# Optimization experiments

Measured on AMD Instinct MI355X. Metric: run time of the kernel, lower is better.

## Reference

```python
import jax, jax.numpy as jnp
import numpy as np

ROTARY_BASE = 10000
INFTY_APPROX = 1e30
B, T, M, H, D = 2, 2048, 2048, 16, 128


def rope(x):
    # x: [B, T, H, D]; half-split rotary encoding
    *_, length, _, width = x.shape
    half = width // 2
    positions = jnp.arange(length, dtype=jnp.float32)[None, :, None, None]      # [1,T,1,1]
    dims = jnp.arange(half, dtype=jnp.float32)
    ang_freqs = jnp.power(float(ROTARY_BASE), -dims / half)[None, None, None, :]  # [1,1,1,D/2]
    radians = positions * ang_freqs
    cos = jnp.cos(radians).astype(x.dtype)
    sin = jnp.sin(radians).astype(x.dtype)
    even, odd = x[..., :half], x[..., half:]
    r_even = even * cos - odd * sin
    r_odd = even * sin + odd * cos
    return jnp.concatenate([r_even, r_odd], axis=-1)


def setup_inputs() -> dict:
    key = jax.random.key(0)
    k0, k1, k2, k3, k4 = jax.random.split(key, 5)
    return {
        "x": jax.random.normal(k0, (B, T, M), dtype=jnp.float32),
        "w_aq": jax.random.normal(k1, (H, M, D), dtype=jnp.float32) * (M ** -0.5),
        "w_ak": jax.random.normal(k2, (H, M, D), dtype=jnp.float32) * (M ** -0.5),
        "w_av": jax.random.normal(k3, (H, M, D), dtype=jnp.float32) * (M ** -0.5),
        "w_ao": jax.random.normal(k4, (H, D, M), dtype=jnp.float32) * ((2 * 24 * M) ** -0.5),
    }


def reference(x, w_aq, w_ak, w_av, w_ao):
    q = jnp.einsum("btm,hmd->bthd", x, w_aq)
    k = jnp.einsum("btm,hmd->bthd", x, w_ak)
    v = jnp.einsum("btm,hmd->bthd", x, w_av)
    q = rope(q)
    k = rope(k)
    # muP attention scaling: 1/d_head (not 1/sqrt(d_head))
    mult = (1.0 / D) ** 0.5
    s = jnp.einsum("bihd,bjhd->bhij", mult * q, mult * k)  # [B,H,T,T]
    i = jnp.arange(T)[:, None]
    j = jnp.arange(T)[None, :]
    mask = (i < j)[None, None, :, :]  # mask future positions
    s = s - jnp.asarray(INFTY_APPROX, dtype=x.dtype) * mask
    p = jax.nn.softmax(s, axis=-1)
    o = jnp.einsum("bhij,bjhd->bihd", p, v)
    r = jnp.einsum("bihd,hdm->bim", o, w_ao)
    return r
```

## Files before the change

### kernel.cpp

```cpp
#include <hip/hip_runtime.h>

#define Bb 2
#define Tt 2048
#define Mm 2048
#define Hh 16
#define Dd 128

typedef __attribute__((ext_vector_type(8))) short bf16x8;
typedef __attribute__((ext_vector_type(4))) float f32x4;
typedef __attribute__((ext_vector_type(16))) float f32x16;

__device__ __forceinline__ unsigned short f2bf(float f) {
    unsigned int u = __builtin_bit_cast(unsigned int, f);
    u += 0x7FFFu + ((u >> 16) & 1u);
    return (unsigned short)(u >> 16);
}

__device__ __forceinline__ unsigned int cvt_pk_bf16(float lo, float hi) {
    unsigned int r;
    asm("v_cvt_pk_bf16_f32 %0, %1, %2" : "=v"(r) : "v"(lo), "v"(hi));
    return r;
}

__device__ __forceinline__ float fexp2(float x) { return __builtin_amdgcn_exp2f(x); }

__device__ __forceinline__ void gld16(const void* g, void* l) {
    __builtin_amdgcn_global_load_lds(
        (const __attribute__((address_space(1))) void*)g,
        (__attribute__((address_space(3))) void*)l, 16, 0, 0);
}


__global__ __launch_bounds__(256) void cvt_x_kernel(const float* __restrict__ x,
                                                    unsigned short* __restrict__ xb) {
    long i = ((long)blockIdx.x * 256 + threadIdx.x) * 4;
    float4 v = *(const float4*)(x + i);
    unsigned short r0 = f2bf(v.x), r1 = f2bf(v.y), r2 = f2bf(v.z), r3 = f2bf(v.w);
    unsigned int lo = (unsigned int)r0 | ((unsigned int)r1 << 16);
    unsigned int hi = (unsigned int)r2 | ((unsigned int)r3 << 16);
    uint2 packed; packed.x = lo; packed.y = hi;
    *(uint2*)(xb + i) = packed;
}

__global__ __launch_bounds__(256) void transpose_cvt(const float* __restrict__ in,
                                                     unsigned short* __restrict__ out,
                                                     int rows, int cols,
                                                     long in_slab, long out_slab) {
    __shared__ float tile[32][33];
    const float* ip = in + (long)blockIdx.z * in_slab;
    unsigned short* op = out + (long)blockIdx.z * out_slab;
    int r0 = blockIdx.x * 32, c0 = blockIdx.y * 32;
    int tx = threadIdx.x & 31, ty = threadIdx.x >> 5;
#pragma unroll
    for (int j = 0; j < 32; j += 8)
        tile[ty + j][tx] = ip[(long)(r0 + ty + j) * cols + c0 + tx];
    __syncthreads();
#pragma unroll
    for (int j = 0; j < 32; j += 8)
        op[(long)(c0 + ty + j) * rows + r0 + tx] = f2bf(tile[tx][ty + j]);
}

__global__ __launch_bounds__(256) void rope_tab(float* __restrict__ cosT,
                                                float* __restrict__ sinT) {
    int idx = blockIdx.x * 256 + threadIdx.x;
    int t = idx >> 6, d = idx & 63;
    float freq = powf(10000.f, -(float)d / 64.f);
    float ang = (float)t * freq;
    sinT[idx] = sinf(ang);
    cosT[idx] = cosf(ang);
}

__global__ __launch_bounds__(256) void proj_gemm(
    const unsigned short* __restrict__ xb,
    const unsigned short* __restrict__ wqT,
    const unsigned short* __restrict__ wkT,
    const unsigned short* __restrict__ wvT,
    unsigned short* __restrict__ qO,
    unsigned short* __restrict__ kO,
    unsigned short* __restrict__ vtO,
    const float* __restrict__ cosT,
    const float* __restrict__ sinT) {
    __shared__ __align__(16) unsigned short smem[32768];

    const int mode = blockIdx.z;
    const unsigned short* wT = (mode == 0) ? wqT : (mode == 1) ? wkT : wvT;
    const int bm = blockIdx.x;
    const int h  = blockIdx.y;
    const int tid = threadIdx.x;
    const int lane = tid & 63;
    const int wave = tid >> 6;
    const int g = lane >> 4;
    const int ln = lane & 15;

    const unsigned short* arow = xb + (long)bm * 128 * Mm;
    const unsigned short* brow = wT + (long)h * 128 * Mm;

    f32x4 acc[2][8];
#pragma unroll
    for (int a = 0; a < 2; ++a)
#pragma unroll
        for (int b2 = 0; b2 < 8; ++b2)
#pragma unroll
            for (int e = 0; e < 4; ++e) acc[a][b2][e] = 0.f;

    auto stage = [&](int buf, int kt) {
        const int k0 = kt * 64;
#pragma unroll
        for (int it = 0; it < 4; ++it) {
            int f = it * 256 + tid;
            int r = f >> 3, c = f & 7;
            long off = (long)r * Mm + k0 + ((c ^ (r & 7)) << 3);
            gld16(arow + off, (char*)smem + buf * 32768 + f * 16);
            gld16(brow + off, (char*)smem + buf * 32768 + 16384 + f * 16);
        }
    };

    stage(0, 0);

    for (int kt = 0; kt < Mm / 64; ++kt) {
        const int cur = kt & 1;
        if (kt + 1 < Mm / 64) {
            stage(cur ^ 1, kt + 1);
            asm volatile("s_waitcnt vmcnt(8)" ::: "memory");
        } else {
            asm volatile("s_waitcnt vmcnt(0)" ::: "memory");
        }
        __builtin_amdgcn_s_barrier();

        const char* Ab = (const char*)smem + cur * 32768;
        const char* Bv = Ab + 16384;
#pragma unroll
        for (int kc = 0; kc < 2; ++kc) {
            bf16x8 af[2];
#pragma unroll
            for (int rf = 0; rf < 2; ++rf) {
                int row = wave * 32 + rf * 16 + ln;
                int byte = (row * 128 + kc * 64 + g * 16) ^ ((row & 7) << 4);
                af[rf] = *(const bf16x8*)(Ab + byte);
            }
#pragma unroll
            for (int ni = 0; ni < 8; ++ni) {
                int row = ni * 16 + ln;
                int byte = (row * 128 + kc * 64 + g * 16) ^ ((row & 7) << 4);
                bf16x8 bfv = *(const bf16x8*)(Bv + byte);
#pragma unroll
                for (int rf = 0; rf < 2; ++rf)
                    acc[rf][ni] = __builtin_amdgcn_mfma_f32_16x16x32_bf16(af[rf], bfv, acc[rf][ni], 0, 0, 0);
            }
        }
        asm volatile("" ::: "memory");
        __builtin_amdgcn_s_barrier();
    }

    const int b  = bm >> 4;
    const int t0 = (bm & 15) * 128;

    if (mode < 2) {
        const float qscale = (mode == 0) ? 0.011271055f : 1.0f;
        unsigned short* out = (mode == 0) ? qO : kO;
        long hb = ((long)(b * Hh + h)) * Tt;
#pragma unroll
        for (int rf = 0; rf < 2; ++rf)
#pragma unroll
            for (int reg = 0; reg < 4; ++reg) {
                int i = wave * 32 + rf * 16 + g * 4 + reg;
                int t = t0 + i;
                long base = (hb + t) * Dd;
#pragma unroll
                for (int ni = 0; ni < 4; ++ni) {
                    int d = ni * 16 + ln;
                    float c = cosT[t * 64 + d];
                    float s = sinT[t * 64 + d];
                    float ev = acc[rf][ni][reg];
                    float od = acc[rf][ni + 4][reg];
                    out[base + d]      = f2bf((ev * c - od * s) * qscale);
                    out[base + d + 64] = f2bf((ev * s + od * c) * qscale);
                }
            }
    } else {
        __syncthreads();
#pragma unroll
        for (int rf = 0; rf < 2; ++rf)
#pragma unroll
            for (int ni = 0; ni < 8; ++ni)
#pragma unroll
                for (int reg = 0; reg < 4; ++reg) {
                    int i = wave * 32 + rf * 16 + g * 4 + reg;
                    int d = ni * 16 + ln;
                    int byte = (d * 256 + i * 2) ^ ((d & 7) << 4);
                    *(unsigned short*)((char*)smem + byte) = f2bf(acc[rf][ni][reg]);
                }
        __syncthreads();
        long hb = ((long)(b * Hh + h)) * Dd;
#pragma unroll
        for (int rep = 0; rep < 8; ++rep) {
            int d = rep * 16 + (tid >> 4);
            int tb = tid & 15;
            int byte = (d * 256 + tb * 16) ^ ((d & 7) << 4);
            uint4 v = *(const uint4*)((char*)smem + byte);
            *(uint4*)(vtO + ((hb + d) * Tt + t0 + tb * 8)) = v;
        }
    }
}

__global__ __launch_bounds__(256) void attn_kernel(
    const unsigned short* __restrict__ q,
    const unsigned short* __restrict__ k,
    const unsigned short* __restrict__ vt,
    unsigned short* __restrict__ o) {
    __shared__ __align__(16) unsigned short lds[32768];

    const int lid = (int)blockIdx.x;
    const int p = lid & 255;
    const int bh = p & 31;
    const int q0 = p >> 5;
    const int qb = (lid >> 8) ? (15 - q0) : q0;

    const int tid = threadIdx.x, lane = tid & 63, wave = tid >> 6;
    const int h = lane >> 5, iln = lane & 31;

    const unsigned short* qp = q + (long)bh * Tt * Dd;
    const unsigned short* kp = k + (long)bh * Tt * Dd;
    const unsigned short* vp = vt + (long)bh * Dd * Tt;

    const int i_g = qb * 128 + wave * 32 + iln;
    bf16x8 qf[8];
#pragma unroll
    for (int kk = 0; kk < 8; ++kk)
        qf[kk] = *(const bf16x8*)(qp + (long)i_g * Dd + kk * 16 + h * 8);

    f32x16 accO[4];
#pragma unroll
    for (int nb = 0; nb < 4; ++nb)
#pragma unroll
        for (int e = 0; e < 16; ++e) accO[nb][e] = 0.f;

    float m_r = -1e30f, l_r = 0.f;

    const int ntiles = 2 * qb + 2;

    auto stage = [&](int buf, int tix) {
        const int j0s = tix * 64;
#pragma unroll
        for (int it = 0; it < 4; ++it) {
            int f = it * 256 + tid;
            int rk = f >> 4, ck = f & 15;
            gld16(kp + ((long)(j0s + rk) * Dd + ((ck ^ (rk & 7)) << 3)),
                  (char*)lds + buf * 16384 + f * 16);
            int rv = f >> 3, cv = f & 7;
            gld16(vp + ((long)rv * Tt + j0s + ((cv ^ (rv & 7)) << 3)),
                  (char*)lds + 32768 + buf * 16384 + f * 16);
        }
    };

    stage(0, 0);

    for (int tix = 0; tix < ntiles; ++tix) {
        const int cur = tix & 1;
        const int j0 = tix * 64;
        if (tix + 1 < ntiles) {
            stage(cur ^ 1, tix + 1);
            asm volatile("s_waitcnt vmcnt(8)" ::: "memory");
        } else {
            asm volatile("s_waitcnt vmcnt(0)" ::: "memory");
        }
        __builtin_amdgcn_s_barrier();

        const char* Kb = (const char*)lds + cur * 16384;
        const char* Vb = (const char*)lds + 32768 + cur * 16384;

        f32x16 sacc[2];
#pragma unroll
        for (int mb = 0; mb < 2; ++mb)
#pragma unroll
            for (int e = 0; e < 16; ++e) sacc[mb][e] = 0.f;

        __builtin_amdgcn_s_setprio(1);
#pragma unroll
        for (int mb = 0; mb < 2; ++mb) {
            int row = mb * 32 + iln;
            const char* Kr = Kb + row * 256;
            int sw = row & 7;
#pragma unroll
            for (int kk = 0; kk < 8; ++kk) {
                bf16x8 kf = *(const bf16x8*)(Kr + 16 * ((kk * 2 + h) ^ sw));
                sacc[mb] = __builtin_amdgcn_mfma_f32_32x32x16_bf16(kf, qf[kk], sacc[mb], 0, 0, 0);
            }
        }
        __builtin_amdgcn_s_setprio(0);

        const bool domask = (j0 + 63 > qb * 128);
        if (domask) {
#pragma unroll
            for (int mb = 0; mb < 2; ++mb)
#pragma unroll
                for (int reg = 0; reg < 16; ++reg) {
                    int j = j0 + mb * 32 + (reg & 3) + 8 * (reg >> 2) + 4 * h;
                    if (j > i_g) sacc[mb][reg] = -1e30f;
                }
        }

        float red[16];
#pragma unroll
        for (int r = 0; r < 16; ++r) red[r] = fmaxf(sacc[0][r], sacc[1][r]);
#pragma unroll
        for (int s = 8; s >= 1; s >>= 1)
#pragma unroll
            for (int r = 0; r < s; ++r) red[r] = fmaxf(red[r], red[r + s]);
        float mx = fmaxf(red[0], __shfl_xor(red[0], 32, 64));

        if (__any(mx > m_r + 8.f)) {
            float mn = fmaxf(m_r, mx);
            float corr = fexp2(m_r - mn);
            m_r = mn;
            l_r *= corr;
#pragma unroll
            for (int reg = 0; reg < 16; ++reg) {
                int rrow = (reg & 3) + 8 * (reg >> 2) + 4 * h;
                float c = __shfl(corr, rrow, 64);
#pragma unroll
                for (int nb = 0; nb < 4; ++nb) accO[nb][reg] *= c;
            }
        }

        float pe[2][16];
#pragma unroll
        for (int mb = 0; mb < 2; ++mb)
#pragma unroll
            for (int r = 0; r < 16; ++r) pe[mb][r] = fexp2(sacc[mb][r] - m_r);
        float sr[16];
#pragma unroll
        for (int r = 0; r < 16; ++r) sr[r] = pe[0][r] + pe[1][r];
#pragma unroll
        for (int s = 8; s >= 1; s >>= 1)
#pragma unroll
            for (int r = 0; r < s; ++r) sr[r] += sr[r + s];
        l_r += sr[0] + __shfl_xor(sr[0], 32, 64);

        unsigned int pu[2][8];
#pragma unroll
        for (int mb = 0; mb < 2; ++mb)
#pragma unroll
            for (int t = 0; t < 8; ++t)
                pu[mb][t] = cvt_pk_bf16(pe[mb][2 * t], pe[mb][2 * t + 1]);

        unsigned int rv[2][4];
#pragma unroll
        for (int mb = 0; mb < 2; ++mb)
#pragma unroll
            for (int u = 0; u < 4; ++u) {
                unsigned int sv = h ? pu[mb][(u & 1) + 4 * (u >> 1)]
                                    : pu[mb][2 + (u & 1) + 4 * (u >> 1)];
                rv[mb][u] = __shfl_xor(sv, 32, 64);
            }

        __builtin_amdgcn_s_setprio(1);
#pragma unroll
        for (int kk2 = 0; kk2 < 4; ++kk2) {
            const int mb = kk2 >> 1, c2 = kk2 & 1;
            unsigned int w0 = h ? rv[mb][2 * c2 + 0] : pu[mb][4 * c2 + 0];
            unsigned int w1 = h ? rv[mb][2 * c2 + 1] : pu[mb][4 * c2 + 1];
            unsigned int w2 = h ? pu[mb][4 * c2 + 2] : rv[mb][2 * c2 + 0];
            unsigned int w3 = h ? pu[mb][4 * c2 + 3] : rv[mb][2 * c2 + 1];
            uint4 aw; aw.x = w0; aw.y = w1; aw.z = w2; aw.w = w3;
            bf16x8 af = __builtin_bit_cast(bf16x8, aw);
#pragma unroll
            for (int nb = 0; nb < 4; ++nb) {
                int d = nb * 32 + iln;
                int byte = d * 128 + 16 * ((kk2 * 2 + h) ^ (d & 7));
                bf16x8 vf = *(const bf16x8*)(Vb + byte);
                accO[nb] = __builtin_amdgcn_mfma_f32_32x32x16_bf16(af, vf, accO[nb], 0, 0, 0);
            }
        }
        __builtin_amdgcn_s_setprio(0);

        asm volatile("" ::: "memory");
        __builtin_amdgcn_s_barrier();
    }

    const int b = bh >> 4, hh = bh & 15;
    float invl = 1.f / l_r;
#pragma unroll
    for (int reg = 0; reg < 16; ++reg) {
        int rrow = (reg & 3) + 8 * (reg >> 2) + 4 * h;
        float iv = __shfl(invl, rrow, 64);
        int t = qb * 128 + wave * 32 + rrow;
        long base = ((long)(b * Tt + t) * Hh + hh) * Dd;
#pragma unroll
        for (int nb = 0; nb < 4; ++nb)
            o[base + nb * 32 + iln] = f2bf(accO[nb][reg] * iv);
    }
}

__global__ __launch_bounds__(256) void out_gemm(
    const unsigned short* __restrict__ oIn,
    const unsigned short* __restrict__ woT,
    float* __restrict__ out) {
    __shared__ __align__(16) unsigned short smem[32768];
    const int bm = blockIdx.x, bn = blockIdx.y;
    const int tid = threadIdx.x;
    const int lane = tid & 63;
    const int wave = tid >> 6;
    const int g = lane >> 4;
    const int ln = lane & 15;

    const unsigned short* arow = oIn + (long)bm * 128 * Mm;
    const unsigned short* brow = woT + (long)bn * 128 * Mm;

    f32x4 acc[2][8];
#pragma unroll
    for (int a = 0; a < 2; ++a)
#pragma unroll
        for (int b2 = 0; b2 < 8; ++b2)
#pragma unroll
            for (int e = 0; e < 4; ++e) acc[a][b2][e] = 0.f;

    auto stage = [&](int buf, int kt) {
        const int k0 = kt * 64;
#pragma unroll
        for (int it = 0; it < 4; ++it) {
            int f = it * 256 + tid;
            int r = f >> 3, c = f & 7;
            long off = (long)r * Mm + k0 + ((c ^ (r & 7)) << 3);
            gld16(arow + off, (char*)smem + buf * 32768 + f * 16);
            gld16(brow + off, (char*)smem + buf * 32768 + 16384 + f * 16);
        }
    };

    stage(0, 0);

    for (int kt = 0; kt < Mm / 64; ++kt) {
        const int cur = kt & 1;
        if (kt + 1 < Mm / 64) {
            stage(cur ^ 1, kt + 1);
            asm volatile("s_waitcnt vmcnt(8)" ::: "memory");
        } else {
            asm volatile("s_waitcnt vmcnt(0)" ::: "memory");
        }
        __builtin_amdgcn_s_barrier();

        const char* Ab = (const char*)smem + cur * 32768;
        const char* Bv = Ab + 16384;
#pragma unroll
        for (int kc = 0; kc < 2; ++kc) {
            bf16x8 af[2];
#pragma unroll
            for (int rf = 0; rf < 2; ++rf) {
                int row = wave * 32 + rf * 16 + ln;
                int byte = (row * 128 + kc * 64 + g * 16) ^ ((row & 7) << 4);
                af[rf] = *(const bf16x8*)(Ab + byte);
            }
#pragma unroll
            for (int ni = 0; ni < 8; ++ni) {
                int row = ni * 16 + ln;
                int byte = (row * 128 + kc * 64 + g * 16) ^ ((row & 7) << 4);
                bf16x8 bfv = *(const bf16x8*)(Bv + byte);
#pragma unroll
                for (int rf = 0; rf < 2; ++rf)
                    acc[rf][ni] = __builtin_amdgcn_mfma_f32_16x16x32_bf16(af[rf], bfv, acc[rf][ni], 0, 0, 0);
            }
        }
        asm volatile("" ::: "memory");
        __builtin_amdgcn_s_barrier();
    }

#pragma unroll
    for (int rf = 0; rf < 2; ++rf)
#pragma unroll
        for (int reg = 0; reg < 4; ++reg) {
            long row = bm * 128 + wave * 32 + rf * 16 + g * 4 + reg;
#pragma unroll
            for (int ni = 0; ni < 8; ++ni)
                out[row * Mm + bn * 128 + ni * 16 + ln] = acc[rf][ni][reg];
        }
}


extern "C" void kernel_launch(void* const* d_in, const int* in_sizes, int n_in,
                              void* d_out, int out_size, void* d_ws, size_t ws_size,
                              hipStream_t stream) {
    const float* x    = (const float*)d_in[0];
    const float* w_aq = (const float*)d_in[1];
    const float* w_ak = (const float*)d_in[2];
    const float* w_av = (const float*)d_in[3];
    const float* w_ao = (const float*)d_in[4];
    float* out = (float*)d_out;

    char* ws = (char*)d_ws;
    const long SZ_BTM = 16777216;
    const long SZ_W   = 8388608;
    unsigned short* xb  = (unsigned short*)(ws);
    unsigned short* qB  = (unsigned short*)(ws + SZ_BTM);
    unsigned short* kB  = (unsigned short*)(ws + 2 * SZ_BTM);
    unsigned short* vtB = (unsigned short*)(ws + 3 * SZ_BTM);
    unsigned short* oB  = (unsigned short*)(ws + 4 * SZ_BTM);
    unsigned short* wqT = (unsigned short*)(ws + 5 * SZ_BTM);
    unsigned short* wkT = (unsigned short*)(ws + 5 * SZ_BTM + SZ_W);
    unsigned short* wvT = (unsigned short*)(ws + 5 * SZ_BTM + 2 * SZ_W);
    unsigned short* woT = (unsigned short*)(ws + 5 * SZ_BTM + 3 * SZ_W);
    float* cosT = (float*)(ws + 5 * SZ_BTM + 4 * SZ_W);
    float* sinT = (float*)(ws + 5 * SZ_BTM + 4 * SZ_W + 524288);

    cvt_x_kernel<<<8192, 256, 0, stream>>>(x, xb);
    transpose_cvt<<<dim3(64, 4, 16), 256, 0, stream>>>(w_aq, wqT, 2048, 128, (long)2048 * 128, (long)128 * 2048);
    transpose_cvt<<<dim3(64, 4, 16), 256, 0, stream>>>(w_ak, wkT, 2048, 128, (long)2048 * 128, (long)128 * 2048);
    transpose_cvt<<<dim3(64, 4, 16), 256, 0, stream>>>(w_av, wvT, 2048, 128, (long)2048 * 128, (long)128 * 2048);
    transpose_cvt<<<dim3(64, 64, 1), 256, 0, stream>>>(w_ao, woT, 2048, 2048, 0, 0);
    rope_tab<<<512, 256, 0, stream>>>(cosT, sinT);

    proj_gemm<<<dim3(32, 16, 3), 256, 0, stream>>>(xb, wqT, wkT, wvT, qB, kB, vtB, cosT, sinT);
    attn_kernel<<<dim3(512), 256, 0, stream>>>(qB, kB, vtB, oB);
    out_gemm<<<dim3(32, 16), 256, 0, stream>>>(oB, woT, out);
}
```

Before: 263.1 us.

## Rewrite QKV projection as 256-row tiles with 512 threads over fused N

Replaces the per-head 128x128 projection GEMM with a 512-thread kernel that computes a 256-row tile against 384 output columns of the concatenated Q/K/V weights, split into 256- and 128-wide subtiles. It uses a two-stage pipeline with 128 KB of LDS and interleaved half-tile loads. The three Q/K/V weight transposes are merged into one launch, and the weight rows are permuted so RoPE even/odd pairs land in matching accumulators. This aims to raise arithmetic intensity and cut A-operand reloads. In exchange it uses far more LDS per block, which limits occupancy, and adds complex indexing and wait-count logic.

Result: faster. 257.7 us (-2.1%).

```diff
diff --git a/kernel.cpp b/kernel.cpp
--- a/kernel.cpp
+++ b/kernel.cpp
@@ -5,6 +5,7 @@
 #define Mm 2048
 #define Hh 16
 #define Dd 128
+#define PROJ_NT 32
 
 typedef __attribute__((ext_vector_type(8))) short bf16x8;
 typedef __attribute__((ext_vector_type(4))) float f32x4;
@@ -60,6 +61,28 @@
         op[(long)(c0 + ty + j) * rows + r0 + tx] = f2bf(tile[tx][ty + j]);
 }
 
+__global__ __launch_bounds__(256) void transpose_cvt_qkv(
+    const float* __restrict__ wq, const float* __restrict__ wk, const float* __restrict__ wv,
+    unsigned short* __restrict__ outBase) {
+    __shared__ float tile[32][33];
+    const int z = blockIdx.z;
+    const int which = z >> 4, slab = z & 15;
+    const float* ip = (which == 0 ? wq : which == 1 ? wk : wv) + (long)slab * 2048 * 128;
+    unsigned short* op = outBase + (long)which * 4194304 + (long)slab * 128 * 2048;
+    int r0 = blockIdx.x * 32, c0 = blockIdx.y * 32;
+    int tx = threadIdx.x & 31, ty = threadIdx.x >> 5;
+#pragma unroll
+    for (int j = 0; j < 32; j += 8)
+        tile[ty + j][tx] = ip[(long)(r0 + ty + j) * 128 + c0 + tx];
+    __syncthreads();
+#pragma unroll
+    for (int j = 0; j < 32; j += 8) {
+        int d = c0 + ty + j;
+        int p = (((d >> 4) & 3) * 2 + (d >> 6)) * 16 + (d & 15);
+        op[(long)p * 2048 + r0 + tx] = f2bf(tile[tx][ty + j]);
+    }
+}
+
 __global__ __launch_bounds__(256) void rope_tab(float* __restrict__ cosT,
                                                 float* __restrict__ sinT) {
     int idx = blockIdx.x * 256 + threadIdx.x;
@@ -70,7 +93,198 @@
     cosT[idx] = cosf(ang);
 }
 
-__global__ __launch_bounds__(256) void proj_gemm(
+template <int BN>
+__device__ __forceinline__ void do_subtile(
+    const unsigned short* __restrict__ Asrc,
+    const unsigned short* __restrict__ Bsrc,
+    char* lds, int mode, int off, int bm,
+    unsigned short* __restrict__ qO, unsigned short* __restrict__ kO,
+    unsigned short* __restrict__ vtO,
+    const float* __restrict__ cosT, const float* __restrict__ sinT,
+    int tid) {
+    const int lane = tid & 63, wave = tid >> 6;
+    const int wm = wave >> 2, wn = wave & 3;
+    const int ln = lane & 15, g4 = lane >> 4;
+    constexpr int NF = BN / 64;
+    constexpr int NQ = (BN == 256) ? 2 : 1;
+
+    f32x4 acc[8][NF];
+#pragma unroll
+    for (int a = 0; a < 8; ++a)
+#pragma unroll
+        for (int b2 = 0; b2 < NF; ++b2)
+#pragma unroll
+            for (int e = 0; e < 4; ++e) acc[a][b2][e] = 0.f;
+
+    auto stA = [&](char* buf, int h, int kt) {
+#pragma unroll
+        for (int l = 0; l < 2; ++l) {
+            int f = l * 512 + tid;
+            int s = ((f >> 9) << 1) + h;
+            int q = f & 511;
+            int r = q >> 3;
+            gld16(Asrc + (long)(s * 64 + r) * Mm + kt * 64 + (((q & 7) ^ (r & 7)) << 3),
+                  buf + s * 8192 + q * 16);
+        }
+    };
+    auto stB = [&](char* buf, int h, int kt) {
+        if constexpr (BN == 256) {
+#pragma unroll
+            for (int l = 0; l < 2; ++l) {
+                int f = l * 512 + tid;
+                int s = ((f >> 8) << 1) + h;
+                int q = f & 255;
+                int r = q >> 3;
+                gld16(Bsrc + (long)(s * 32 + r) * Mm + kt * 64 + (((q & 7) ^ (r & 7)) << 3),
+                      buf + 32768 + s * 4096 + q * 16);
+            }
+        } else {
+            int f = tid;
+            int s = ((f >> 7) << 1) + h;
+            int q = f & 127;
+            int r = q >> 3;
+            gld16(Bsrc + (long)(s * 16 + r) * Mm + kt * 64 + (((q & 7) ^ (r & 7)) << 3),
+                  buf + 32768 + s * 2048 + q * 16);
+        }
+    };
+
+    auto rdA = [&](const char* buf, int MH, int mf, int kk) -> bf16x8 {
+        int row = wm * 128 + MH * 64 + mf * 16 + ln;
+        int byte = (row >> 6) * 8192 + ((((row & 63) * 128) + (kk * 4 + g4) * 16) ^ ((row & 7) << 4));
+        return *(const bf16x8*)(buf + byte);
+    };
+    auto rdB = [&](const char* buf, int NH, int nf, int kk) -> bf16x8 {
+        if constexpr (BN == 256) {
+            int col = wn * 64 + NH * 32 + nf * 16 + ln;
+            int byte = 32768 + (col >> 5) * 4096 +
+                       ((((col & 31) * 128) + (kk * 4 + g4) * 16) ^ ((col & 7) << 4));
+            return *(const bf16x8*)(buf + byte);
+        } else {
+            int col = wn * 32 + NH * 16 + ln;
+            int byte = 32768 + (col >> 4) * 2048 +
+                       ((((col & 15) * 128) + (kk * 4 + g4) * 16) ^ ((col & 7) << 4));
+            return *(const bf16x8*)(buf + byte);
+        }
+    };
+
+    auto phase = [&](const char* bc, int MH, int NH) {
+        bf16x8 af[4][2];
+#pragma unroll
+        for (int mf = 0; mf < 4; ++mf)
+#pragma unroll
+            for (int kk = 0; kk < 2; ++kk) af[mf][kk] = rdA(bc, MH, mf, kk);
+        bf16x8 bfr[NQ][2];
+#pragma unroll
+        for (int nf = 0; nf < NQ; ++nf)
+#pragma unroll
+            for (int kk = 0; kk < 2; ++kk) bfr[nf][kk] = rdB(bc, NH, nf, kk);
+        __builtin_amdgcn_s_setprio(1);
+#pragma unroll
+        for (int mf = 0; mf < 4; ++mf)
+#pragma unroll
+            for (int nf = 0; nf < NQ; ++nf)
+#pragma unroll
+                for (int kk = 0; kk < 2; ++kk)
+                    acc[MH * 4 + mf][NH * NQ + nf] = __builtin_amdgcn_mfma_f32_16x16x32_bf16(
+                        af[mf][kk], bfr[nf][kk], acc[MH * 4 + mf][NH * NQ + nf], 0, 0, 0);
+        __builtin_amdgcn_s_setprio(0);
+    };
+
+    stB(lds, 0, 0); stA(lds, 1, 0); stA(lds, 0, 0); stB(lds, 1, 0);
+    stB(lds + 65536, 0, 1); stA(lds + 65536, 1, 1);
+
+    for (int t = 0; t < PROJ_NT; ++t) {
+        char* bc = lds + (t & 1) * 65536;
+        char* bo = lds + (((t & 1) ^ 1) * 65536);
+        const int tn1 = (t + 1 < PROJ_NT) ? t + 1 : PROJ_NT - 1;
+        const int tn2 = (t + 2 < PROJ_NT) ? t + 2 : PROJ_NT - 1;
+
+        stA(bo, 0, tn1);
+        if constexpr (BN == 256) asm volatile("s_waitcnt vmcnt(8)" ::: "memory");
+        else                     asm volatile("s_waitcnt vmcnt(6)" ::: "memory");
+        asm volatile("s_barrier" ::: "memory");
+        phase(bc, 0, 0);
+        asm volatile("s_barrier" ::: "memory");
+
+        stB(bo, 1, tn1);
+        asm volatile("s_barrier" ::: "memory");
+        phase(bc, 1, 0);
+        asm volatile("s_barrier" ::: "memory");
+
+        stB(bc, 0, tn2);
+        if constexpr (BN == 256) asm volatile("s_waitcnt vmcnt(10)" ::: "memory");
+        else                     asm volatile("s_waitcnt vmcnt(7)" ::: "memory");
+        asm volatile("s_barrier" ::: "memory");
+        phase(bc, 1, 1);
+        asm volatile("s_barrier" ::: "memory");
+
+        stA(bc, 1, tn2);
+        asm volatile("s_barrier" ::: "memory");
+        phase(bc, 0, 1);
+        asm volatile("s_barrier" ::: "memory");
+    }
+    asm volatile("s_waitcnt vmcnt(0)" ::: "memory");
+    __syncthreads();
+
+    const int b = bm >> 3;
+    const int t0w = (bm & 7) * 256 + wm * 128;
+    const int headL = (off & 2047) >> 7;
+
+    if (mode < 2) {
+        const float qs = (mode == 0) ? 0.011271055f : 1.0f;
+        unsigned short* out = (mode == 0) ? qO : kO;
+#pragma unroll
+        for (int MF = 0; MF < 8; ++MF)
+#pragma unroll
+            for (int NP = 0; NP < NF; NP += 2) {
+                int head, j16;
+                if constexpr (BN == 256) { head = headL + (wn >> 1); j16 = (wn & 1) * 2 + (NP >> 1); }
+                else                     { head = headL; j16 = wn; }
+                int dlo = j16 * 16 + ln;
+#pragma unroll
+                for (int e = 0; e < 4; ++e) {
+                    int t = t0w + MF * 16 + g4 * 4 + e;
+                    float c = cosT[t * 64 + dlo], s = sinT[t * 64 + dlo];
+                    float ev = acc[MF][NP][e], od = acc[MF][NP + 1][e];
+                    long base = (((long)(b * Hh + head)) * Tt + t) * Dd;
+                    out[base + dlo]      = f2bf((ev * c - od * s) * qs);
+                    out[base + dlo + 64] = f2bf((ev * s + od * c) * qs);
+                }
+            }
+    } else {
+        constexpr int PS = (BN == 256) ? 16384 : 8192;
+        char* patch = lds + wave * PS;
+#pragma unroll
+        for (int MF = 0; MF < 8; ++MF)
+#pragma unroll
+            for (int NFi = 0; NFi < NF; ++NFi) {
+                int dslot = NFi * 16 + ln;
+#pragma unroll
+                for (int e = 0; e < 4; ++e) {
+                    int tloc = MF * 16 + g4 * 4 + e;
+                    int byte = (dslot * 256 + tloc * 2) ^ ((dslot & 7) << 4);
+                    *(unsigned short*)(patch + byte) = f2bf(acc[MF][NFi][e]);
+                }
+            }
+        constexpr int NPASS = (BN == 256) ? 16 : 8;
+#pragma unroll
+        for (int p = 0; p < NPASS; ++p) {
+            int dslot = p * 4 + g4;
+            int t8 = ln;
+            int byte = (dslot * 256 + t8 * 16) ^ ((dslot & 7) << 4);
+            uint4 v = *(const uint4*)(patch + byte);
+            int NFi = dslot >> 4;
+            int head, j16;
+            if constexpr (BN == 256) { head = headL + (wn >> 1); j16 = (wn & 1) * 2 + (NFi >> 1); }
+            else                     { head = headL; j16 = wn; }
+            int d = (NFi & 1) * 64 + j16 * 16 + (dslot & 15);
+            long baseo = (((long)(b * Hh + head)) * Dd + d) * Tt + t0w + t8 * 8;
+            *(uint4*)(vtO + baseo) = v;
+        }
+    }
+}
+
+__global__ __launch_bounds__(512, 2) void proj_gemm2(
     const unsigned short* __restrict__ xb,
     const unsigned short* __restrict__ wqT,
     const unsigned short* __restrict__ wkT,
@@ -80,126 +294,27 @@
     unsigned short* __restrict__ vtO,
     const float* __restrict__ cosT,
     const float* __restrict__ sinT) {
-    __shared__ __align__(16) unsigned short smem[32768];
-
-    const int mode = blockIdx.z;
-    const unsigned short* wT = (mode == 0) ? wqT : (mode == 1) ? wkT : wvT;
-    const int bm = blockIdx.x;
-    const int h  = blockIdx.y;
+    __shared__ __align__(16) char lds[131072];
+    const int bm = blockIdx.x, bn = blockIdx.y;
     const int tid = threadIdx.x;
-    const int lane = tid & 63;
-    const int wave = tid >> 6;
-    const int g = lane >> 4;
-    const int ln = lane & 15;
-
-    const unsigned short* arow = xb + (long)bm * 128 * Mm;
-    const unsigned short* brow = wT + (long)h * 128 * Mm;
-
-    f32x4 acc[2][8];
-#pragma unroll
-    for (int a = 0; a < 2; ++a)
-#pragma unroll
-        for (int b2 = 0; b2 < 8; ++b2)
-#pragma unroll
-            for (int e = 0; e < 4; ++e) acc[a][b2][e] = 0.f;
-
-    auto stage = [&](int buf, int kt) {
-        const int k0 = kt * 64;
-#pragma unroll
-        for (int it = 0; it < 4; ++it) {
-            int f = it * 256 + tid;
-            int r = f >> 3, c = f & 7;
-            long off = (long)r * Mm + k0 + ((c ^ (r & 7)) << 3);
-            gld16(arow + off, (char*)smem + buf * 32768 + f * 16);
-            gld16(brow + off, (char*)smem + buf * 32768 + 16384 + f * 16);
-        }
-    };
-
-    stage(0, 0);
-
-    for (int kt = 0; kt < Mm / 64; ++kt) {
-        const int cur = kt & 1;
-        if (kt + 1 < Mm / 64) {
-            stage(cur ^ 1, kt + 1);
-            asm volatile("s_waitcnt vmcnt(8)" ::: "memory");
-        } else {
-            asm volatile("s_waitcnt vmcnt(0)" ::: "memory");
-        }
-        __builtin_amdgcn_s_barrier();
-
-        const char* Ab = (const char*)smem + cur * 32768;
-        const char* Bv = Ab + 16384;
-#pragma unroll
-        for (int kc = 0; kc < 2; ++kc) {
-            bf16x8 af[2];
-#pragma unroll
-            for (int rf = 0; rf < 2; ++rf) {
-                int row = wave * 32 + rf * 16 + ln;
-                int byte = (row * 128 + kc * 64 + g * 16) ^ ((row & 7) << 4);
-                af[rf] = *(const bf16x8*)(Ab + byte);
-            }
-#pragma unroll
-            for (int ni = 0; ni < 8; ++ni) {
-                int row = ni * 16 + ln;
-                int byte = (row * 128 + kc * 64 + g * 16) ^ ((row & 7) << 4);
-                bf16x8 bfv = *(const bf16x8*)(Bv + byte);
-#pragma unroll
-                for (int rf = 0; rf < 2; ++rf)
-                    acc[rf][ni] = __builtin_amdgcn_mfma_f32_16x16x32_bf16(af[rf], bfv, acc[rf][ni], 0, 0, 0);
-            }
-        }
-        asm volatile("" ::: "memory");
-        __builtin_amdgcn_s_barrier();
-    }
-
-    const int b  = bm >> 4;
-    const int t0 = (bm & 15) * 128;
-
-    if (mode < 2) {
-        const float qscale = (mode == 0) ? 0.011271055f : 1.0f;
-        unsigned short* out = (mode == 0) ? qO : kO;
-        long hb = ((long)(b * Hh + h)) * Tt;
-#pragma unroll
-        for (int rf = 0; rf < 2; ++rf)
-#pragma unroll
-            for (int reg = 0; reg < 4; ++reg) {
-                int i = wave * 32 + rf * 16 + g * 4 + reg;
-                int t = t0 + i;
-                long base = (hb + t) * Dd;
-#pragma unroll
-                for (int ni = 0; ni < 4; ++ni) {
-                    int d = ni * 16 + ln;
-                    float c = cosT[t * 64 + d];
-                    float s = sinT[t * 64 + d];
-                    float ev = acc[rf][ni][reg];
-                    float od = acc[rf][ni + 4][reg];
-                    out[base + d]      = f2bf((ev * c - od * s) * qscale);
-                    out[base + d + 64] = f2bf((ev * s + od * c) * qscale);
-                }
-            }
-    } else {
-        __syncthreads();
-#pragma unroll
-        for (int rf = 0; rf < 2; ++rf)
-#pragma unroll
-            for (int ni = 0; ni < 8; ++ni)
-#pragma unroll
-                for (int reg = 0; reg < 4; ++reg) {
-                    int i = wave * 32 + rf * 16 + g * 4 + reg;
-                    int d = ni * 16 + ln;
-                    int byte = (d * 256 + i * 2) ^ ((d & 7) << 4);
-                    *(unsigned short*)((char*)smem + byte) = f2bf(acc[rf][ni][reg]);
-                }
-        __syncthreads();
-        long hb = ((long)(b * Hh + h)) * Dd;
-#pragma unroll
-        for (int rep = 0; rep < 8; ++rep) {
-            int d = rep * 16 + (tid >> 4);
-            int tb = tid & 15;
-            int byte = (d * 256 + tb * 16) ^ ((d & 7) << 4);
-            uint4 v = *(const uint4*)((char*)smem + byte);
-            *(uint4*)(vtO + ((hb + d) * Tt + t0 + tb * 8)) = v;
-        }
+    const int s = bn * 384;
+    const bool swap = ((s & 2047) == 1920);
+    const int offw = swap ? s + 128 : s;
+    const int offn = swap ? s : s + 256;
+    const unsigned short* Asrc = xb + (long)bm * 256 * Mm;
+
+    {
+        int mode = offw >> 11;
+        const unsigned short* wT = (mode == 0) ? wqT : (mode == 1) ? wkT : wvT;
+        do_subtile<256>(Asrc, wT + (long)(offw & 2047) * Mm, lds, mode, offw, bm,
+                        qO, kO, vtO, cosT, sinT, tid);
+    }
+    __syncthreads();
+    {
+        int mode = offn >> 11;
+        const unsigned short* wT = (mode == 0) ? wqT : (mode == 1) ? wkT : wvT;
+        do_subtile<128>(Asrc, wT + (long)(offn & 2047) * Mm, lds, mode, offn, bm,
+                        qO, kO, vtO, cosT, sinT, tid);
     }
 }
 
@@ -236,7 +351,6 @@
         for (int e = 0; e < 16; ++e) accO[nb][e] = 0.f;
 
     float m_r = -1e30f, l_r = 0.f;
-
     const int ntiles = 2 * qb + 2;
 
     auto stage = [&](int buf, int tix) {
@@ -344,24 +458,24 @@
             for (int t = 0; t < 8; ++t)
                 pu[mb][t] = cvt_pk_bf16(pe[mb][2 * t], pe[mb][2 * t + 1]);
 
-        unsigned int rv[2][4];
+        unsigned int rv2[2][4];
 #pragma unroll
         for (int mb = 0; mb < 2; ++mb)
 #pragma unroll
             for (int u = 0; u < 4; ++u) {
                 unsigned int sv = h ? pu[mb][(u & 1) + 4 * (u >> 1)]
                                     : pu[mb][2 + (u & 1) + 4 * (u >> 1)];
-                rv[mb][u] = __shfl_xor(sv, 32, 64);
+                rv2[mb][u] = __shfl_xor(sv, 32, 64);
             }
 
         __builtin_amdgcn_s_setprio(1);
 #pragma unroll
         for (int kk2 = 0; kk2 < 4; ++kk2) {
             const int mb = kk2 >> 1, c2 = kk2 & 1;
-            unsigned int w0 = h ? rv[mb][2 * c2 + 0] : pu[mb][4 * c2 + 0];
-            unsigned int w1 = h ? rv[mb][2 * c2 + 1] : pu[mb][4 * c2 + 1];
-            unsigned int w2 = h ? pu[mb][4 * c2 + 2] : rv[mb][2 * c2 + 0];
-            unsigned int w3 = h ? pu[mb][4 * c2 + 3] : rv[mb][2 * c2 + 1];
+            unsigned int w0 = h ? rv2[mb][2 * c2 + 0] : pu[mb][4 * c2 + 0];
+            unsigned int w1 = h ? rv2[mb][2 * c2 + 1] : pu[mb][4 * c2 + 1];
+            unsigned int w2 = h ? pu[mb][4 * c2 + 2] : rv2[mb][2 * c2 + 0];
+            unsigned int w3 = h ? pu[mb][4 * c2 + 3] : rv2[mb][2 * c2 + 1];
             uint4 aw; aw.x = w0; aw.y = w1; aw.z = w2; aw.w = w3;
             bf16x8 af = __builtin_bit_cast(bf16x8, aw);
 #pragma unroll
@@ -502,13 +616,11 @@
     float* sinT = (float*)(ws + 5 * SZ_BTM + 4 * SZ_W + 524288);
 
     cvt_x_kernel<<<8192, 256, 0, stream>>>(x, xb);
-    transpose_cvt<<<dim3(64, 4, 16), 256, 0, stream>>>(w_aq, wqT, 2048, 128, (long)2048 * 128, (long)128 * 2048);
-    transpose_cvt<<<dim3(64, 4, 16), 256, 0, stream>>>(w_ak, wkT, 2048, 128, (long)2048 * 128, (long)128 * 2048);
-    transpose_cvt<<<dim3(64, 4, 16), 256, 0, stream>>>(w_av, wvT, 2048, 128, (long)2048 * 128, (long)128 * 2048);
+    transpose_cvt_qkv<<<dim3(64, 4, 48), 256, 0, stream>>>(w_aq, w_ak, w_av, wqT);
     transpose_cvt<<<dim3(64, 64, 1), 256, 0, stream>>>(w_ao, woT, 2048, 2048, 0, 0);
     rope_tab<<<512, 256, 0, stream>>>(cosT, sinT);
 
-    proj_gemm<<<dim3(32, 16, 3), 256, 0, stream>>>(xb, wqT, wkT, wvT, qB, kB, vtB, cosT, sinT);
+    proj_gemm2<<<dim3(16, 16), 512, 0, stream>>>(xb, wqT, wkT, wvT, qB, kB, vtB, cosT, sinT);
     attn_kernel<<<dim3(512), 256, 0, stream>>>(qB, kB, vtB, oB);
     out_gemm<<<dim3(32, 16), 256, 0, stream>>>(oB, woT, out);
 }
```

## Rework QKV and output GEMMs with 32x32 MFMA tiles and fused weight transpose

Applied to the files above, without the earlier changes.

The QKV projection becomes a 128x256 tile kernel covering two heads per block. It uses 32x32x16 MFMA on a 2x2 wave grid, and the weight transpose reorders D rows so the rotary halves land in matching fragments. The three QKV weight transposes merge into one launch. The output GEMM also switches to 32x32x16 MFMA with a 2x2 wave layout and requests two blocks per CU. Both GEMMs drop the double-buffered prefetch for a single-buffer load, wait and compute loop. That removes global-load and compute overlap in exchange for fewer LDS reads per MFMA and higher occupancy.

Result: slower. 276.3 us (+5.0%).

```diff
diff --git a/kernel.cpp b/kernel.cpp
--- a/kernel.cpp
+++ b/kernel.cpp
@@ -60,6 +60,29 @@
         op[(long)(c0 + ty + j) * rows + r0 + tx] = f2bf(tile[tx][ty + j]);
 }
 
+__global__ __launch_bounds__(256) void transpose_cvt_qkv(
+    const float* __restrict__ wq, const float* __restrict__ wk, const float* __restrict__ wv,
+    unsigned short* __restrict__ outBase) {
+    __shared__ float tile[32][33];
+    const int z = blockIdx.z;
+    const int which = z >> 4, slab = z & 15;
+    const float* ip = (which == 0 ? wq : which == 1 ? wk : wv) + (long)slab * 2048 * 128;
+    unsigned short* op = outBase + (long)which * 4194304 + (long)slab * 128 * 2048;
+    int r0 = blockIdx.x * 32, c0 = blockIdx.y * 32;
+    int tx = threadIdx.x & 31, ty = threadIdx.x >> 5;
+#pragma unroll
+    for (int j = 0; j < 32; j += 8)
+        tile[ty + j][tx] = ip[(long)(r0 + ty + j) * 128 + c0 + tx];
+    __syncthreads();
+#pragma unroll
+    for (int j = 0; j < 32; j += 8) {
+        int d = c0 + ty + j;
+        int ord = (d >> 6) + 2 * ((d >> 5) & 1);
+        int p = (d & 31) + 32 * ord;
+        op[(long)p * 2048 + r0 + tx] = f2bf(tile[tx][ty + j]);
+    }
+}
+
 __global__ __launch_bounds__(256) void rope_tab(float* __restrict__ cosT,
                                                 float* __restrict__ sinT) {
     int idx = blockIdx.x * 256 + threadIdx.x;
@@ -70,7 +93,7 @@
     cosT[idx] = cosf(ang);
 }
 
-__global__ __launch_bounds__(256) void proj_gemm(
+__global__ __launch_bounds__(256, 2) void proj_gemm3(
     const unsigned short* __restrict__ xb,
     const unsigned short* __restrict__ wqT,
     const unsigned short* __restrict__ wkT,
@@ -80,125 +103,123 @@
     unsigned short* __restrict__ vtO,
     const float* __restrict__ cosT,
     const float* __restrict__ sinT) {
-    __shared__ __align__(16) unsigned short smem[32768];
-
-    const int mode = blockIdx.z;
+    __shared__ __align__(16) char lds[49152];
+    const int bm = blockIdx.x;
+    const int bn = blockIdx.y;
+    const int off = bn * 256;
+    const int mode = off >> 11;
     const unsigned short* wT = (mode == 0) ? wqT : (mode == 1) ? wkT : wvT;
-    const int bm = blockIdx.x;
-    const int h  = blockIdx.y;
-    const int tid = threadIdx.x;
-    const int lane = tid & 63;
-    const int wave = tid >> 6;
-    const int g = lane >> 4;
-    const int ln = lane & 15;
-
-    const unsigned short* arow = xb + (long)bm * 128 * Mm;
-    const unsigned short* brow = wT + (long)h * 128 * Mm;
-
-    f32x4 acc[2][8];
+    const unsigned short* Asrc = xb + (long)bm * 128 * Mm;
+    const unsigned short* Bsrc = wT + (long)(off & 2047) * Mm;
+
+    const int tid = threadIdx.x, lane = tid & 63, wave = tid >> 6;
+    const int il = lane & 31, hl = lane >> 5;
+    const int wm = wave >> 1, wn = wave & 1;
+
+    f32x16 acc[2][4];
 #pragma unroll
     for (int a = 0; a < 2; ++a)
 #pragma unroll
-        for (int b2 = 0; b2 < 8; ++b2)
-#pragma unroll
-            for (int e = 0; e < 4; ++e) acc[a][b2][e] = 0.f;
-
-    auto stage = [&](int buf, int kt) {
-        const int k0 = kt * 64;
-#pragma unroll
-        for (int it = 0; it < 4; ++it) {
-            int f = it * 256 + tid;
+        for (int b2 = 0; b2 < 4; ++b2)
+#pragma unroll
+            for (int e = 0; e < 16; ++e) acc[a][b2][e] = 0.f;
+
+    for (int kt = 0; kt < 32; ++kt) {
+#pragma unroll
+        for (int l = 0; l < 4; ++l) {
+            int f = l * 256 + tid;
             int r = f >> 3, c = f & 7;
-            long off = (long)r * Mm + k0 + ((c ^ (r & 7)) << 3);
-            gld16(arow + off, (char*)smem + buf * 32768 + f * 16);
-            gld16(brow + off, (char*)smem + buf * 32768 + 16384 + f * 16);
-        }
-    };
-
-    stage(0, 0);
-
-    for (int kt = 0; kt < Mm / 64; ++kt) {
-        const int cur = kt & 1;
-        if (kt + 1 < Mm / 64) {
-            stage(cur ^ 1, kt + 1);
-            asm volatile("s_waitcnt vmcnt(8)" ::: "memory");
-        } else {
-            asm volatile("s_waitcnt vmcnt(0)" ::: "memory");
-        }
+            gld16(Asrc + (long)r * Mm + kt * 64 + ((c ^ (r & 7)) << 3), lds + f * 16);
+        }
+#pragma unroll
+        for (int l = 0; l < 8; ++l) {
+            int f = l * 256 + tid;
+            int s = f >> 8, q = f & 255, rr = q >> 3, c = q & 7;
+            gld16(Bsrc + (long)(s * 32 + rr) * Mm + kt * 64 + ((c ^ (rr & 7)) << 3),
+                  lds + 16384 + f * 16);
+        }
+        asm volatile("s_waitcnt vmcnt(0)" ::: "memory");
         __builtin_amdgcn_s_barrier();
 
-        const char* Ab = (const char*)smem + cur * 32768;
-        const char* Bv = Ab + 16384;
-#pragma unroll
-        for (int kc = 0; kc < 2; ++kc) {
-            bf16x8 af[2];
-#pragma unroll
-            for (int rf = 0; rf < 2; ++rf) {
-                int row = wave * 32 + rf * 16 + ln;
-                int byte = (row * 128 + kc * 64 + g * 16) ^ ((row & 7) << 4);
-                af[rf] = *(const bf16x8*)(Ab + byte);
-            }
-#pragma unroll
-            for (int ni = 0; ni < 8; ++ni) {
-                int row = ni * 16 + ln;
-                int byte = (row * 128 + kc * 64 + g * 16) ^ ((row & 7) << 4);
-                bf16x8 bfv = *(const bf16x8*)(Bv + byte);
-#pragma unroll
-                for (int rf = 0; rf < 2; ++rf)
-                    acc[rf][ni] = __builtin_amdgcn_mfma_f32_16x16x32_bf16(af[rf], bfv, acc[rf][ni], 0, 0, 0);
-            }
+#pragma unroll
+        for (int kk = 0; kk < 4; ++kk) {
+            bf16x8 af[2], bf[4];
+#pragma unroll
+            for (int mf = 0; mf < 2; ++mf) {
+                int row = wm * 64 + mf * 32 + il;
+                af[mf] = *(const bf16x8*)(lds + row * 128 + (((kk * 2 + hl) ^ (row & 7)) << 4));
+            }
+#pragma unroll
+            for (int nf = 0; nf < 4; ++nf) {
+                int st = wn * 4 + nf;
+                bf[nf] = *(const bf16x8*)(lds + 16384 + st * 4096 + il * 128 +
+                                          (((kk * 2 + hl) ^ (il & 7)) << 4));
+            }
+            __builtin_amdgcn_s_setprio(1);
+#pragma unroll
+            for (int mf = 0; mf < 2; ++mf)
+#pragma unroll
+                for (int nf = 0; nf < 4; ++nf)
+                    acc[mf][nf] = __builtin_amdgcn_mfma_f32_32x32x16_bf16(af[mf], bf[nf], acc[mf][nf], 0, 0, 0);
+            __builtin_amdgcn_s_setprio(0);
         }
         asm volatile("" ::: "memory");
         __builtin_amdgcn_s_barrier();
     }
 
-    const int b  = bm >> 4;
+    const int b = bm >> 4;
     const int t0 = (bm & 15) * 128;
+    const int head = ((off & 2047) >> 7) + wn;
 
     if (mode < 2) {
-        const float qscale = (mode == 0) ? 0.011271055f : 1.0f;
-        unsigned short* out = (mode == 0) ? qO : kO;
-        long hb = ((long)(b * Hh + h)) * Tt;
-#pragma unroll
-        for (int rf = 0; rf < 2; ++rf)
-#pragma unroll
-            for (int reg = 0; reg < 4; ++reg) {
-                int i = wave * 32 + rf * 16 + g * 4 + reg;
-                int t = t0 + i;
-                long base = (hb + t) * Dd;
-#pragma unroll
-                for (int ni = 0; ni < 4; ++ni) {
-                    int d = ni * 16 + ln;
-                    float c = cosT[t * 64 + d];
-                    float s = sinT[t * 64 + d];
-                    float ev = acc[rf][ni][reg];
-                    float od = acc[rf][ni + 4][reg];
-                    out[base + d]      = f2bf((ev * c - od * s) * qscale);
-                    out[base + d + 64] = f2bf((ev * s + od * c) * qscale);
+        const float qs = (mode == 0) ? 0.011271055f : 1.0f;
+        unsigned short* outp = (mode == 0) ? qO : kO;
+        long hb = ((long)(b * Hh + head)) * Tt;
+#pragma unroll
+        for (int mf = 0; mf < 2; ++mf)
+#pragma unroll
+            for (int np = 0; np < 2; ++np) {
+                int d_lo = il + 32 * np;
+#pragma unroll
+                for (int reg = 0; reg < 16; ++reg) {
+                    int r = (reg & 3) + 8 * (reg >> 2) + 4 * hl;
+                    int t = t0 + wm * 64 + mf * 32 + r;
+                    float c = cosT[t * 64 + d_lo], s = sinT[t * 64 + d_lo];
+                    float ev = acc[mf][np * 2][reg], od = acc[mf][np * 2 + 1][reg];
+                    long base = (hb + t) * Dd;
+                    outp[base + d_lo]      = f2bf((ev * c - od * s) * qs);
+                    outp[base + d_lo + 64] = f2bf((ev * s + od * c) * qs);
                 }
             }
     } else {
-        __syncthreads();
-#pragma unroll
-        for (int rf = 0; rf < 2; ++rf)
-#pragma unroll
-            for (int ni = 0; ni < 8; ++ni)
-#pragma unroll
-                for (int reg = 0; reg < 4; ++reg) {
-                    int i = wave * 32 + rf * 16 + g * 4 + reg;
-                    int d = ni * 16 + ln;
-                    int byte = (d * 256 + i * 2) ^ ((d & 7) << 4);
-                    *(unsigned short*)((char*)smem + byte) = f2bf(acc[rf][ni][reg]);
+        char* patch = lds + wave * 8192;
+        long hdbase = ((long)(b * Hh + head)) * Dd;
+#pragma unroll
+        for (int mf = 0; mf < 2; ++mf) {
+#pragma unroll
+            for (int nf = 0; nf < 4; ++nf) {
+                int dslot = nf * 32 + il;
+                int swz = (dslot & 3) << 4;
+#pragma unroll
+                for (int qg = 0; qg < 4; ++qg) {
+                    uint2 w;
+                    w.x = cvt_pk_bf16(acc[mf][nf][qg * 4 + 0], acc[mf][nf][qg * 4 + 1]);
+                    w.y = cvt_pk_bf16(acc[mf][nf][qg * 4 + 2], acc[mf][nf][qg * 4 + 3]);
+                    *(uint2*)(patch + dslot * 64 + ((qg * 16 + hl * 8) ^ swz)) = w;
                 }
-        __syncthreads();
-        long hb = ((long)(b * Hh + h)) * Dd;
-#pragma unroll
-        for (int rep = 0; rep < 8; ++rep) {
-            int d = rep * 16 + (tid >> 4);
-            int tb = tid & 15;
-            int byte = (d * 256 + tb * 16) ^ ((d & 7) << 4);
-            uint4 v = *(const uint4*)((char*)smem + byte);
-            *(uint4*)(vtO + ((hb + d) * Tt + t0 + tb * 8)) = v;
+            }
+            __builtin_amdgcn_s_waitcnt(0);
+#pragma unroll
+            for (int p = 0; p < 8; ++p) {
+                int dslot = p * 16 + (lane >> 2);
+                int t8 = lane & 3;
+                uint4 v = *(const uint4*)(patch + dslot * 64 + ((t8 * 16) ^ ((dslot & 3) << 4)));
+                int ordv = dslot >> 5, il2 = dslot & 31;
+                int d = il2 + 32 * (ordv >> 1) + 64 * (ordv & 1);
+                int tg = t0 + wm * 64 + mf * 32 + t8 * 8;
+                *(uint4*)(vtO + (hdbase + d) * Tt + tg) = v;
+            }
+            __builtin_amdgcn_s_waitcnt(0);
         }
     }
 }
@@ -236,7 +257,6 @@
         for (int e = 0; e < 16; ++e) accO[nb][e] = 0.f;
 
     float m_r = -1e30f, l_r = 0.f;
-
     const int ntiles = 2 * qb + 2;
 
     auto stage = [&](int buf, int tix) {
@@ -344,24 +364,24 @@
             for (int t = 0; t < 8; ++t)
                 pu[mb][t] = cvt_pk_bf16(pe[mb][2 * t], pe[mb][2 * t + 1]);
 
-        unsigned int rv[2][4];
+        unsigned int rv2[2][4];
 #pragma unroll
         for (int mb = 0; mb < 2; ++mb)
 #pragma unroll
             for (int u = 0; u < 4; ++u) {
                 unsigned int sv = h ? pu[mb][(u & 1) + 4 * (u >> 1)]
                                     : pu[mb][2 + (u & 1) + 4 * (u >> 1)];
-                rv[mb][u] = __shfl_xor(sv, 32, 64);
+                rv2[mb][u] = __shfl_xor(sv, 32, 64);
             }
 
         __builtin_amdgcn_s_setprio(1);
 #pragma unroll
         for (int kk2 = 0; kk2 < 4; ++kk2) {
             const int mb = kk2 >> 1, c2 = kk2 & 1;
-            unsigned int w0 = h ? rv[mb][2 * c2 + 0] : pu[mb][4 * c2 + 0];
-            unsigned int w1 = h ? rv[mb][2 * c2 + 1] : pu[mb][4 * c2 + 1];
-            unsigned int w2 = h ? pu[mb][4 * c2 + 2] : rv[mb][2 * c2 + 0];
-            unsigned int w3 = h ? pu[mb][4 * c2 + 3] : rv[mb][2 * c2 + 1];
+            unsigned int w0 = h ? rv2[mb][2 * c2 + 0] : pu[mb][4 * c2 + 0];
+            unsigned int w1 = h ? rv2[mb][2 * c2 + 1] : pu[mb][4 * c2 + 1];
+            unsigned int w2 = h ? pu[mb][4 * c2 + 2] : rv2[mb][2 * c2 + 0];
+            unsigned int w3 = h ? pu[mb][4 * c2 + 3] : rv2[mb][2 * c2 + 1];
             uint4 aw; aw.x = w0; aw.y = w1; aw.z = w2; aw.w = w3;
             bf16x8 af = __builtin_bit_cast(bf16x8, aw);
 #pragma unroll
@@ -392,87 +412,76 @@
     }
 }
 
-__global__ __launch_bounds__(256) void out_gemm(
+__global__ __launch_bounds__(256, 2) void out_gemm3(
     const unsigned short* __restrict__ oIn,
     const unsigned short* __restrict__ woT,
     float* __restrict__ out) {
-    __shared__ __align__(16) unsigned short smem[32768];
+    __shared__ __align__(16) char lds[32768];
     const int bm = blockIdx.x, bn = blockIdx.y;
-    const int tid = threadIdx.x;
-    const int lane = tid & 63;
-    const int wave = tid >> 6;
-    const int g = lane >> 4;
-    const int ln = lane & 15;
-
-    const unsigned short* arow = oIn + (long)bm * 128 * Mm;
-    const unsigned short* brow = woT + (long)bn * 128 * Mm;
-
-    f32x4 acc[2][8];
+    const int tid = threadIdx.x, lane = tid & 63, wave = tid >> 6;
+    const int il = lane & 31, hl = lane >> 5;
+    const int wm = wave >> 1, wn = wave & 1;
+
+    const unsigned short* Asrc = oIn + (long)bm * 128 * Mm;
+    const unsigned short* Bsrc = woT + (long)bn * 128 * Mm;
+
+    f32x16 acc[2][2];
 #pragma unroll
     for (int a = 0; a < 2; ++a)
 #pragma unroll
-        for (int b2 = 0; b2 < 8; ++b2)
-#pragma unroll
-            for (int e = 0; e < 4; ++e) acc[a][b2][e] = 0.f;
-
-    auto stage = [&](int buf, int kt) {
-        const int k0 = kt * 64;
-#pragma unroll
-        for (int it = 0; it < 4; ++it) {
-            int f = it * 256 + tid;
+        for (int b2 = 0; b2 < 2; ++b2)
+#pragma unroll
+            for (int e = 0; e < 16; ++e) acc[a][b2][e] = 0.f;
+
+    for (int kt = 0; kt < 32; ++kt) {
+#pragma unroll
+        for (int l = 0; l < 4; ++l) {
+            int f = l * 256 + tid;
             int r = f >> 3, c = f & 7;
-            long off = (long)r * Mm + k0 + ((c ^ (r & 7)) << 3);
-            gld16(arow + off, (char*)smem + buf * 32768 + f * 16);
-            gld16(brow + off, (char*)smem + buf * 32768 + 16384 + f * 16);
-        }
-    };
-
-    stage(0, 0);
-
-    for (int kt = 0; kt < Mm / 64; ++kt) {
-        const int cur = kt & 1;
-        if (kt + 1 < Mm / 64) {
-            stage(cur ^ 1, kt + 1);
-            asm volatile("s_waitcnt vmcnt(8)" ::: "memory");
-        } else {
-            asm volatile("s_waitcnt vmcnt(0)" ::: "memory");
-        }
+            long koff = kt * 64 + ((c ^ (r & 7)) << 3);
+            gld16(Asrc + (long)r * Mm + koff, lds + f * 16);
+            gld16(Bsrc + (long)r * Mm + koff, lds + 16384 + f * 16);
+        }
+        asm volatile("s_waitcnt vmcnt(0)" ::: "memory");
         __builtin_amdgcn_s_barrier();
 
-        const char* Ab = (const char*)smem + cur * 32768;
-        const char* Bv = Ab + 16384;
-#pragma unroll
-        for (int kc = 0; kc < 2; ++kc) {
-            bf16x8 af[2];
-#pragma unroll
-            for (int rf = 0; rf < 2; ++rf) {
-                int row = wave * 32 + rf * 16 + ln;
-                int byte = (row * 128 + kc * 64 + g * 16) ^ ((row & 7) << 4);
-                af[rf] = *(const bf16x8*)(Ab + byte);
-            }
-#pragma unroll
-            for (int ni = 0; ni < 8; ++ni) {
-                int row = ni * 16 + ln;
-                int byte = (row * 128 + kc * 64 + g * 16) ^ ((row & 7) << 4);
-                bf16x8 bfv = *(const bf16x8*)(Bv + byte);
-#pragma unroll
-                for (int rf = 0; rf < 2; ++rf)
-                    acc[rf][ni] = __builtin_amdgcn_mfma_f32_16x16x32_bf16(af[rf], bfv, acc[rf][ni], 0, 0, 0);
-            }
+#pragma unroll
+        for (int kk = 0; kk < 4; ++kk) {
+            bf16x8 af[2], bf[2];
+#pragma unroll
+            for (int mf = 0; mf < 2; ++mf) {
+                int row = wm * 64 + mf * 32 + il;
+                af[mf] = *(const bf16x8*)(lds + row * 128 + (((kk * 2 + hl) ^ (row & 7)) << 4));
+            }
+#pragma unroll
+            for (int nf = 0; nf < 2; ++nf) {
+                int col = wn * 64 + nf * 32 + il;
+                bf[nf] = *(const bf16x8*)(lds + 16384 + col * 128 +
+                                          (((kk * 2 + hl) ^ (col & 7)) << 4));
+            }
+            __builtin_amdgcn_s_setprio(1);
+#pragma unroll
+            for (int mf = 0; mf < 2; ++mf)
+#pragma unroll
+                for (int nf = 0; nf < 2; ++nf)
+                    acc[mf][nf] = __builtin_amdgcn_mfma_f32_32x32x16_bf16(af[mf], bf[nf], acc[mf][nf], 0, 0, 0);
+            __builtin_amdgcn_s_setprio(0);
         }
         asm volatile("" ::: "memory");
         __builtin_amdgcn_s_barrier();
     }
 
 #pragma unroll
-    for (int rf = 0; rf < 2; ++rf)
-#pragma unroll
-        for (int reg = 0; reg < 4; ++reg) {
-            long row = bm * 128 + wave * 32 + rf * 16 + g * 4 + reg;
-#pragma unroll
-            for (int ni = 0; ni < 8; ++ni)
-                out[row * Mm + bn * 128 + ni * 16 + ln] = acc[rf][ni][reg];
-        }
+    for (int mf = 0; mf < 2; ++mf)
+#pragma unroll
+        for (int nf = 0; nf < 2; ++nf)
+#pragma unroll
+            for (int reg = 0; reg < 16; ++reg) {
+                int r = (reg & 3) + 8 * (reg >> 2) + 4 * hl;
+                long row = bm * 128 + wm * 64 + mf * 32 + r;
+                int col = bn * 128 + wn * 64 + nf * 32 + il;
+                out[row * Mm + col] = acc[mf][nf][reg];
+            }
 }
 
 
@@ -502,13 +511,11 @@
     float* sinT = (float*)(ws + 5 * SZ_BTM + 4 * SZ_W + 524288);
 
     cvt_x_kernel<<<8192, 256, 0, stream>>>(x, xb);
-    transpose_cvt<<<dim3(64, 4, 16), 256, 0, stream>>>(w_aq, wqT, 2048, 128, (long)2048 * 128, (long)128 * 2048);
-    transpose_cvt<<<dim3(64, 4, 16), 256, 0, stream>>>(w_ak, wkT, 2048, 128, (long)2048 * 128, (long)128 * 2048);
-    transpose_cvt<<<dim3(64, 4, 16), 256, 0, stream>>>(w_av, wvT, 2048, 128, (long)2048 * 128, (long)128 * 2048);
+    transpose_cvt_qkv<<<dim3(64, 4, 48), 256, 0, stream>>>(w_aq, w_ak, w_av, wqT);
     transpose_cvt<<<dim3(64, 64, 1), 256, 0, stream>>>(w_ao, woT, 2048, 2048, 0, 0);
     rope_tab<<<512, 256, 0, stream>>>(cosT, sinT);
 
-    proj_gemm<<<dim3(32, 16, 3), 256, 0, stream>>>(xb, wqT, wkT, wvT, qB, kB, vtB, cosT, sinT);
+    proj_gemm3<<<dim3(32, 24), 256, 0, stream>>>(xb, wqT, wkT, wvT, qB, kB, vtB, cosT, sinT);
     attn_kernel<<<dim3(512), 256, 0, stream>>>(qB, kB, vtB, oB);
-    out_gemm<<<dim3(32, 16), 256, 0, stream>>>(oB, woT, out);
-}
+    out_gemm3<<<dim3(32, 16), 256, 0, stream>>>(oB, woT, out);
+}
```
